# Kernel optimization log

Hardware: AMD Instinct MI355X
Metric: run time of the kernel (lower is better)

## Reference

```python
import jax, jax.numpy as jnp
import numpy as np

H = 512
IN_CH = 3
DIM = 32
FILTER_SIZES = [4, 4, 2]
OUT_DIM = 1
BATCH = 128


def _patchify(x, f):
    # (B, C, D, D) -> (B, C, P, P, f*f) non-overlapping patches (matches torch unfold+reshape)
    B, C, D, _ = x.shape
    P = D // f
    xp = x.reshape(B, C, P, f, P, f).transpose(0, 1, 2, 4, 3, 5)
    return xp.reshape(B, C, P, P, f * f)


def _loc_block(x, w, f):
    # w: (O, C, P, P, f*f) -- per-patch unshared filters
    C = x.shape[1]
    xp = _patchify(x, f)
    y = jnp.einsum('bcpqf,ocpqf->bopq', xp, w)
    return jax.nn.relu(y / (f * f * C) ** 0.5)


def setup_inputs() -> dict:
    key = jax.random.key(0)
    ks = jax.random.split(key, 5)
    f1, f2, f3 = FILTER_SIZES
    P1 = DIM // f1            # 8
    P2 = P1 // f2             # 2
    P3 = P2 // f3             # 1
    x = jax.random.normal(ks[0], (BATCH, IN_CH, DIM, DIM), dtype=jnp.float32)
    w1 = jax.random.normal(ks[1], (H, IN_CH, P1, P1, f1 * f1), dtype=jnp.float32)
    w2 = jax.random.normal(ks[2], (H, H, P2, P2, f2 * f2), dtype=jnp.float32)
    w3 = jax.random.normal(ks[3], (H, H, P3, P3, f3 * f3), dtype=jnp.float32)
    beta = jax.random.normal(ks[4], (H * P3 * P3, OUT_DIM), dtype=jnp.float32)
    return {'x': x, 'w1': w1, 'w2': w2, 'w3': w3, 'beta': beta}


def reference(x, w1, w2, w3, beta):
    f1, f2, f3 = FILTER_SIZES
    y = _loc_block(x, w1, f1)
    y = _loc_block(y, w2, f2)
    y = _loc_block(y, w3, f3)
    y = y.reshape(y.shape[0], -1)
    return y @ beta / beta.shape[0] ** 0.5
```

## Files before the change

### kernel.cpp

```cpp
#include <hip/hip_runtime.h>


typedef _Float16 f16;
typedef _Float16 half8 __attribute__((ext_vector_type(8)));
typedef _Float16 half4 __attribute__((ext_vector_type(4)));
typedef float f32x4 __attribute__((ext_vector_type(4)));

#define SWZ(r, c) ((((r) << 6) + (c)) ^ (((r) & 7) << 3))
#define SWZL(r, c) ((((r) << 10) + (c)) ^ (((r) & 7) << 3))

#define GLOAD_LDS16(G, L)                                                     \
  __builtin_amdgcn_global_load_lds(                                           \
      (const __attribute__((address_space(1))) void*)(G),                     \
      (__attribute__((address_space(3))) void*)(L), 16, 0, 0)

__global__ __launch_bounds__(256) void l1_mfma(const float* __restrict__ x,
                                               const float* __restrict__ w1,
                                               f16* __restrict__ A2) {
  const int o0 = blockIdx.x << 5;
  const int s2 = blockIdx.y;
  const int b0 = blockIdx.z << 5;
  const int p2 = s2 >> 1, q2 = s2 & 1;
  __shared__ __align__(16) f16 Xs[32 * 1024];
  __shared__ __align__(16) f16 Ws[32 * 1024];
  const int t = threadIdx.x;
#pragma unroll
  for (int i = 0; i < 8; ++i) {
    int e = (i << 8) + t;
    int row = e >> 6, rem = e & 63, g = rem >> 2, j = rem & 3;
    half4 z = {};
    *(half4*)&Xs[SWZL(row, g * 64 + 48 + j * 4)] = z;
    *(half4*)&Ws[SWZL(row, g * 64 + 48 + j * 4)] = z;
  }
#pragma unroll
  for (int i = 0; i < 24; ++i) {
    int fl = (i << 8) + t;
    int b = fl / 192, rem = fl % 192;
    int c = rem >> 6, rem2 = rem & 63;
    int a = rem2 >> 4, fi = (rem2 >> 2) & 3, bq = rem2 & 3;
    float4 v = *(const float4*)(x + ((size_t)(b0 + b) * 3 + c) * 1024 +
                                (p2 * 16 + a * 4 + fi) * 32 + q2 * 16 + bq * 4);
    half4 h;
    h[0] = (f16)v.x; h[1] = (f16)v.y; h[2] = (f16)v.z; h[3] = (f16)v.w;
    *(half4*)&Xs[SWZL(b, (a * 4 + bq) * 64 + c * 16 + fi * 4)] = h;
  }
#pragma unroll
  for (int i = 0; i < 24; ++i) {
    int fl = (i << 8) + t;
    int o = fl / 192, rem = fl % 192;
    int c = rem >> 6, rem2 = rem & 63;
    int g = rem2 >> 2, f4 = rem2 & 3;
    float4 v = *(const float4*)(w1 + (size_t)(o0 + o) * 3072 + c * 1024 +
                                (p2 * 4 + (g >> 2)) * 128 + (q2 * 4 + (g & 3)) * 16 + f4 * 4);
    half4 h;
    h[0] = (f16)v.x; h[1] = (f16)v.y; h[2] = (f16)v.z; h[3] = (f16)v.w;
    *(half4*)&Ws[SWZL(o, g * 64 + c * 16 + f4 * 4)] = h;
  }
  __syncthreads();

  const int wv = t >> 6, ln = t & 63;
  const int bw = wv >> 1, ow = wv & 1;
  const int frow = ln & 15, fr4 = ln >> 4;
  f32x4 acc[16] = {};
#pragma unroll
  for (int g = 0; g < 16; ++g) {
#pragma unroll
    for (int ks = 0; ks < 2; ++ks) {
      half8 a = *(const half8*)&Xs[SWZL(bw * 16 + frow, g * 64 + ks * 32 + fr4 * 8)];
      half8 b = *(const half8*)&Ws[SWZL(ow * 16 + frow, g * 64 + ks * 32 + fr4 * 8)];
      acc[g] = __builtin_amdgcn_mfma_f32_16x16x32_f16(a, b, acc[g], 0, 0, 0);
    }
  }
  f16* A2b = A2 + (size_t)s2 * 128 * 8192;
#pragma unroll
  for (int r = 0; r < 4; ++r) {
    int b = b0 + bw * 16 + fr4 * 4 + r;
    int o = o0 + ow * 16 + frow;
    f16 tmp[16];
#pragma unroll
    for (int g = 0; g < 16; ++g)
      tmp[g] = (f16)fmaxf(acc[g][r] * 0.14433756729740643f, 0.f);
    f16* dst = A2b + (size_t)b * 8192 + o * 16;
    *(half8*)dst = *(half8*)&tmp[0];
    *(half8*)(dst + 8) = *(half8*)&tmp[8];
  }
}

__global__ __launch_bounds__(512) void gemm0(const f16* __restrict__ A,
                                             const float* __restrict__ W,
                                             f16* __restrict__ P) {
  __shared__ __align__(16) f16 As[2][128 * 64];
  __shared__ __align__(16) float Bs[2][128 * 64];
  const int t = threadIdx.x;
  const int bid = blockIdx.x;
  constexpr int AK = 8192, ITERS = 8;
  const int s = bid >> 6;
  const int kc = (bid >> 2) & 15;
  const int n = bid & 3;
  const int kb0 = kc * (ITERS * 64);
  const f16* Ab = A + (size_t)s * 128 * AK + kb0;
  const int o0 = n << 7;

  const int wv = t >> 6, ln = t & 63;

#define STAGE(IT, BUF)                                                          \
  {                                                                             \
    _Pragma("unroll") for (int jj = 0; jj < 2; ++jj) {                          \
      int rbase = wv * 16 + jj * 8;                                             \
      int r = rbase + (ln >> 3);                                                \
      int sg = (ln & 7) ^ (r & 7);                                              \
      GLOAD_LDS16(Ab + (size_t)r * AK + ((IT) << 6) + (sg << 3),                \
                  &As[BUF][rbase << 6]);                                        \
    }                                                                           \
    _Pragma("unroll") for (int jj = 0; jj < 4; ++jj) {                          \
      int rbase = wv * 16 + jj * 4;                                             \
      int r = rbase + (ln >> 4);                                                \
      int sg = (ln & 15) ^ (r & 7);                                             \
      int k = kb0 + ((IT) << 6) + (sg << 2);                                    \
      const float* gp = W + (size_t)(o0 + r) * 32768 + ((k >> 4) << 6) +        \
                        (s << 4) + (k & 15);                                    \
      GLOAD_LDS16(gp, &Bs[BUF][rbase << 6]);                                    \
    }                                                                           \
  }

  const int wr = wv >> 2, wc = wv & 3;
  const int frow = ln & 15, fr4 = ln >> 4;
  f32x4 acc[4][2] = {};

#define COMPUTE(BUF)                                                            \
  _Pragma("unroll") for (int ks = 0; ks < 2; ++ks) {                            \
    half8 a[4];                                                                 \
    _Pragma("unroll") for (int mi = 0; mi < 4; ++mi) {                          \
      int r = wr * 64 + mi * 16 + frow;                                         \
      int gl = ((ks << 2) + fr4) ^ (r & 7);                                     \
      a[mi] = *(const half8*)&As[BUF][(r << 6) + (gl << 3)];                    \
    }                                                                           \
    _Pragma("unroll") for (int ni = 0; ni < 2; ++ni) {                          \
      int r = wc * 32 + ni * 16 + frow;                                         \
      int s0 = (ks << 3) + (fr4 << 1);                                          \
      float4 f0 = *(const float4*)&Bs[BUF][(r << 6) + ((s0 ^ (r & 7)) << 2)];   \
      float4 f1 = *(const float4*)&Bs[BUF][(r << 6) + (((s0 + 1) ^ (r & 7)) << 2)]; \
      half8 hb;                                                                 \
      hb[0] = (f16)f0.x; hb[1] = (f16)f0.y; hb[2] = (f16)f0.z; hb[3] = (f16)f0.w; \
      hb[4] = (f16)f1.x; hb[5] = (f16)f1.y; hb[6] = (f16)f1.z; hb[7] = (f16)f1.w; \
      _Pragma("unroll") for (int mi = 0; mi < 4; ++mi)                          \
        acc[mi][ni] = __builtin_amdgcn_mfma_f32_16x16x32_f16(a[mi], hb, acc[mi][ni], 0, 0, 0); \
    }                                                                           \
  }

  STAGE(0, 0)
#pragma unroll
  for (int it = 0; it < ITERS; ++it) {
    const int cur = it & 1;
    if (it + 1 < ITERS) {
      STAGE(it + 1, cur ^ 1)
      asm volatile("s_waitcnt vmcnt(6)" ::: "memory");
    } else {
      asm volatile("s_waitcnt vmcnt(0)" ::: "memory");
    }
    __builtin_amdgcn_s_barrier();
    __builtin_amdgcn_sched_barrier(0);
    COMPUTE(cur)
    __builtin_amdgcn_sched_barrier(0);
    __builtin_amdgcn_s_barrier();
  }

  f16* Pb = P + (size_t)((kc << 2) + s) * 65536;
#pragma unroll
  for (int mi = 0; mi < 4; ++mi)
#pragma unroll
    for (int ni = 0; ni < 2; ++ni)
#pragma unroll
      for (int r = 0; r < 4; ++r) {
        int gm = wr * 64 + mi * 16 + fr4 * 4 + r;
        int gn = o0 + wc * 32 + ni * 16 + frow;
        Pb[(size_t)gm * 512 + gn] = (f16)acc[mi][ni][r];
      }
#undef STAGE
#undef COMPUTE
}

__global__ __launch_bounds__(256) void gemm1(const f16* __restrict__ A,
                                             const float* __restrict__ W,
                                             f16* __restrict__ P) {
  __shared__ __align__(16) f16 As[2][128 * 64];
  __shared__ __align__(16) float Bs[2][64 * 64];
  const int t = threadIdx.x;
  const int bid = blockIdx.x;
  constexpr int AK = 2048, ITERS = 2;
  const int kc = bid >> 3;
  const int n = bid & 7;
  const int kb0 = kc * (ITERS * 64);
  const f16* Ab = A + kb0;
  const int o0 = n << 6;
  const int wv = t >> 6, ln = t & 63;
  const int a_r = (ln >> 3), a_sg0 = ln & 7;
  const int b_r = (ln >> 4), b_sg0 = ln & 15;

#define STAGE(IT, BUF)                                                          \
  {                                                                             \
    _Pragma("unroll") for (int jj = 0; jj < 4; ++jj) {                          \
      int rbase = wv * 32 + jj * 8;                                             \
      int r = rbase + a_r;                                                      \
      int sg = a_sg0 ^ (r & 7);                                                 \
      GLOAD_LDS16(Ab + (size_t)r * AK + ((IT) << 6) + (sg << 3),                \
                  &As[BUF][rbase << 6]);                                        \
    }                                                                           \
    _Pragma("unroll") for (int jj = 0; jj < 4; ++jj) {                          \
      int rbase = wv * 16 + jj * 4;                                             \
      int r = rbase + b_r;                                                      \
      int sg = b_sg0 ^ (r & 7);                                                 \
      const float* gp = W + (size_t)(o0 + r) * 2048 + kb0 + ((IT) << 6) + (sg << 2); \
      GLOAD_LDS16(gp, &Bs[BUF][rbase << 6]);                                    \
    }                                                                           \
  }

  const int wr = wv >> 1, wc = wv & 1;
  const int frow = ln & 15, fr4 = ln >> 4;
  f32x4 acc[4][2] = {};

#define COMPUTE(BUF)                                                            \
  _Pragma("unroll") for (int ks = 0; ks < 2; ++ks) {                            \
    half8 a[4];                                                                 \
    _Pragma("unroll") for (int mi = 0; mi < 4; ++mi) {                          \
      int r = wr * 64 + mi * 16 + frow;                                         \
      int gl = ((ks << 2) + fr4) ^ (r & 7);                                     \
      a[mi] = *(const half8*)&As[BUF][(r << 6) + (gl << 3)];                    \
    }                                                                           \
    _Pragma("unroll") for (int ni = 0; ni < 2; ++ni) {                          \
      int r = wc * 32 + ni * 16 + frow;                                         \
      int s0 = (ks << 3) + (fr4 << 1);                                          \
      float4 f0 = *(const float4*)&Bs[BUF][(r << 6) + ((s0 ^ (r & 7)) << 2)];   \
      float4 f1 = *(const float4*)&Bs[BUF][(r << 6) + (((s0 + 1) ^ (r & 7)) << 2)]; \
      half8 hb;                                                                 \
      hb[0] = (f16)f0.x; hb[1] = (f16)f0.y; hb[2] = (f16)f0.z; hb[3] = (f16)f0.w; \
      hb[4] = (f16)f1.x; hb[5] = (f16)f1.y; hb[6] = (f16)f1.z; hb[7] = (f16)f1.w; \
      _Pragma("unroll") for (int mi = 0; mi < 4; ++mi)                          \
        acc[mi][ni] = __builtin_amdgcn_mfma_f32_16x16x32_f16(a[mi], hb, acc[mi][ni], 0, 0, 0); \
    }                                                                           \
  }

  STAGE(0, 0)
#pragma unroll
  for (int it = 0; it < ITERS; ++it) {
    const int cur = it & 1;
    if (it + 1 < ITERS) {
      STAGE(it + 1, cur ^ 1)
      asm volatile("s_waitcnt vmcnt(8)" ::: "memory");
    } else {
      asm volatile("s_waitcnt vmcnt(0)" ::: "memory");
    }
    __builtin_amdgcn_s_barrier();
    __builtin_amdgcn_sched_barrier(0);
    COMPUTE(cur)
    __builtin_amdgcn_sched_barrier(0);
    __builtin_amdgcn_s_barrier();
  }

  f16* Pb = P + (size_t)kc * 65536;
#pragma unroll
  for (int mi = 0; mi < 4; ++mi)
#pragma unroll
    for (int ni = 0; ni < 2; ++ni)
#pragma unroll
      for (int r = 0; r < 4; ++r) {
        int gm = wr * 64 + mi * 16 + fr4 * 4 + r;
        int gn = o0 + wc * 32 + ni * 16 + frow;
        Pb[(size_t)gm * 512 + gn] = (f16)acc[mi][ni][r];
      }
#undef STAGE
#undef COMPUTE
}

__global__ __launch_bounds__(256) void reduce2(const f16* __restrict__ P2,
                                               f16* __restrict__ A3) {
  int idx = blockIdx.x * 256 + threadIdx.x;
  int og = idx & 127, b = idx >> 7;
  f16 outv[16];
#pragma unroll
  for (int s = 0; s < 4; ++s) {
    float a0 = 0.f, a1 = 0.f, a2 = 0.f, a3 = 0.f;
#pragma unroll
    for (int kc = 0; kc < 16; ++kc) {
      half4 v = *(const half4*)(P2 + (size_t)((kc << 2) + s) * 65536 + b * 512 + og * 4);
      a0 += (float)v[0]; a1 += (float)v[1]; a2 += (float)v[2]; a3 += (float)v[3];
    }
    outv[0 * 4 + s] = (f16)fmaxf(a0 * 0.011048543456039805f, 0.f);
    outv[1 * 4 + s] = (f16)fmaxf(a1 * 0.011048543456039805f, 0.f);
    outv[2 * 4 + s] = (f16)fmaxf(a2 * 0.011048543456039805f, 0.f);
    outv[3 * 4 + s] = (f16)fmaxf(a3 * 0.011048543456039805f, 0.f);
  }
  f16* dst = A3 + (size_t)b * 2048 + og * 16;
  *(half8*)dst = *(half8*)&outv[0];
  *(half8*)(dst + 8) = *(half8*)&outv[8];
}

__global__ __launch_bounds__(256) void out_fused(const f16* __restrict__ P3,
                                                 const float* __restrict__ beta,
                                                 float* __restrict__ out) {
  __shared__ float red[4];
  const int b = blockIdx.x, t = threadIdx.x;
  float acc = 0.f;
#pragma unroll
  for (int oi = 0; oi < 2; ++oi) {
    int o = (oi << 8) + t;
    float v = 0.f;
#pragma unroll
    for (int kc = 0; kc < 16; ++kc) v += (float)P3[(size_t)kc * 65536 + b * 512 + o];
    acc += fmaxf(v * 0.022097086912079608f, 0.f) * beta[o];
  }
#pragma unroll
  for (int off = 32; off > 0; off >>= 1) acc += __shfl_down(acc, off);
  if ((t & 63) == 0) red[t >> 6] = acc;
  __syncthreads();
  if (t == 0) out[b] = (red[0] + red[1] + red[2] + red[3]) * 0.044194173824159216f;
}

extern "C" void kernel_launch(void* const* d_in, const int* in_sizes, int n_in,
                              void* d_out, int out_size, void* d_ws, size_t ws_size,
                              hipStream_t stream) {
  const float* x    = (const float*)d_in[0];
  const float* w1   = (const float*)d_in[1];
  const float* w2   = (const float*)d_in[2];
  const float* w3   = (const float*)d_in[3];
  const float* beta = (const float*)d_in[4];
  float* out = (float*)d_out;

  char* wsb = (char*)d_ws;
  f16* A2 = (f16*)wsb;
  f16* P2 = (f16*)(wsb + (8ull << 20));
  f16* A3 = (f16*)(wsb + (16ull << 20));
  f16* P3 = (f16*)(wsb + (16ull << 20) + (1ull << 19));

  l1_mfma<<<dim3(16, 4, 4), 256, 0, stream>>>(x, w1, A2);
  gemm0<<<256, 512, 0, stream>>>(A2, w2, P2);
  reduce2<<<64, 256, 0, stream>>>(P2, A3);
  gemm1<<<128, 256, 0, stream>>>(A3, w3, P3);
  out_fused<<<128, 256, 0, stream>>>(P3, beta, out);
}
```

Before: 44.98 us.

## Stage gemm0 B weights via registers with fp16 conversion before LDS write

gemm0 used to DMA fp32 weights straight into LDS and convert them to fp16 inside the MFMA inner loop. Now each thread loads the weights as float4 into registers, converts them to half4 once, and writes them into a swizzled fp16 LDS buffer after the compute of the current stage. This halves the LDS footprint of B and takes the conversion out of the per-MFMA path, and launch bounds add an occupancy hint. The cost is extra VGPRs for the staged registers and a register round-trip that may overlap less well with compute than the direct-to-LDS DMA did.

```diff
diff --git a/kernel.cpp b/kernel.cpp
--- a/kernel.cpp
+++ b/kernel.cpp
@@ -86,41 +86,50 @@
   }
 }
 
-__global__ __launch_bounds__(512) void gemm0(const f16* __restrict__ A,
-                                             const float* __restrict__ W,
-                                             f16* __restrict__ P) {
+__global__ __launch_bounds__(512, 4) void gemm0(const f16* __restrict__ A,
+                                                const float* __restrict__ W,
+                                                f16* __restrict__ P) {
   __shared__ __align__(16) f16 As[2][128 * 64];
-  __shared__ __align__(16) float Bs[2][128 * 64];
+  __shared__ __align__(16) f16 Bs[2][128 * 64];
   const int t = threadIdx.x;
   const int bid = blockIdx.x;
   constexpr int AK = 8192, ITERS = 8;
   const int s = bid >> 6;
   const int kc = (bid >> 2) & 15;
   const int n = bid & 3;
-  const int kb0 = kc * (ITERS * 64);
+  const int kb0 = kc * 512;
   const f16* Ab = A + (size_t)s * 128 * AK + kb0;
   const int o0 = n << 7;
 
   const int wv = t >> 6, ln = t & 63;
-
-#define STAGE(IT, BUF)                                                          \
-  {                                                                             \
-    _Pragma("unroll") for (int jj = 0; jj < 2; ++jj) {                          \
-      int rbase = wv * 16 + jj * 8;                                             \
-      int r = rbase + (ln >> 3);                                                \
-      int sg = (ln & 7) ^ (r & 7);                                              \
-      GLOAD_LDS16(Ab + (size_t)r * AK + ((IT) << 6) + (sg << 3),                \
-                  &As[BUF][rbase << 6]);                                        \
-    }                                                                           \
-    _Pragma("unroll") for (int jj = 0; jj < 4; ++jj) {                          \
-      int rbase = wv * 16 + jj * 4;                                             \
-      int r = rbase + (ln >> 4);                                                \
-      int sg = (ln & 15) ^ (r & 7);                                             \
-      int k = kb0 + ((IT) << 6) + (sg << 2);                                    \
-      const float* gp = W + (size_t)(o0 + r) * 32768 + ((k >> 4) << 6) +        \
-                        (s << 4) + (k & 15);                                    \
-      GLOAD_LDS16(gp, &Bs[BUF][rbase << 6]);                                    \
-    }                                                                           \
+  const int br = t >> 4, bslot = t & 15;
+  float4 breg[4];
+
+#define B_LOAD(IT)                                                              \
+  _Pragma("unroll") for (int i = 0; i < 4; ++i) {                               \
+    int r = i * 32 + br;                                                        \
+    int k = kb0 + ((IT) << 6) + (bslot << 2);                                   \
+    breg[i] = *(const float4*)(W + (size_t)(o0 + r) * 32768 + ((k >> 4) << 6) + \
+                               (s << 4) + (k & 15));                            \
+  }
+
+#define A_DMA(IT, BUF)                                                          \
+  _Pragma("unroll") for (int jj = 0; jj < 2; ++jj) {                            \
+    int rbase = wv * 16 + jj * 8;                                               \
+    int r = rbase + (ln >> 3);                                                  \
+    int sg = (ln & 7) ^ (r & 7);                                                \
+    GLOAD_LDS16(Ab + (size_t)r * AK + ((IT) << 6) + (sg << 3),                  \
+                &As[BUF][rbase << 6]);                                          \
+  }
+
+#define B_WRITE(BUF)                                                            \
+  _Pragma("unroll") for (int i = 0; i < 4; ++i) {                               \
+    int r = i * 32 + br;                                                        \
+    half4 h4;                                                                   \
+    h4[0] = (f16)breg[i].x; h4[1] = (f16)breg[i].y;                             \
+    h4[2] = (f16)breg[i].z; h4[3] = (f16)breg[i].w;                             \
+    int off = (r << 6) + (((bslot >> 1) ^ (r & 7)) << 3) + ((bslot & 1) << 2);  \
+    *(half4*)&Bs[BUF][off] = h4;                                                \
   }
 
   const int wr = wv >> 2, wc = wv & 3;
@@ -137,31 +146,35 @@
     }                                                                           \
     _Pragma("unroll") for (int ni = 0; ni < 2; ++ni) {                          \
       int r = wc * 32 + ni * 16 + frow;                                         \
-      int s0 = (ks << 3) + (fr4 << 1);                                          \
-      float4 f0 = *(const float4*)&Bs[BUF][(r << 6) + ((s0 ^ (r & 7)) << 2)];   \
-      float4 f1 = *(const float4*)&Bs[BUF][(r << 6) + (((s0 + 1) ^ (r & 7)) << 2)]; \
-      half8 hb;                                                                 \
-      hb[0] = (f16)f0.x; hb[1] = (f16)f0.y; hb[2] = (f16)f0.z; hb[3] = (f16)f0.w; \
-      hb[4] = (f16)f1.x; hb[5] = (f16)f1.y; hb[6] = (f16)f1.z; hb[7] = (f16)f1.w; \
+      int gl = ((ks << 2) + fr4) ^ (r & 7);                                     \
+      half8 hb = *(const half8*)&Bs[BUF][(r << 6) + (gl << 3)];                 \
       _Pragma("unroll") for (int mi = 0; mi < 4; ++mi)                          \
         acc[mi][ni] = __builtin_amdgcn_mfma_f32_16x16x32_f16(a[mi], hb, acc[mi][ni], 0, 0, 0); \
     }                                                                           \
   }
 
-  STAGE(0, 0)
+  B_LOAD(0)
+  A_DMA(0, 0)
+  asm volatile("s_waitcnt vmcnt(2)" ::: "memory");
+  B_WRITE(0)
 #pragma unroll
   for (int it = 0; it < ITERS; ++it) {
     const int cur = it & 1;
     if (it + 1 < ITERS) {
-      STAGE(it + 1, cur ^ 1)
-      asm volatile("s_waitcnt vmcnt(6)" ::: "memory");
+      B_LOAD(it + 1)
+      A_DMA(it + 1, cur ^ 1)
+      asm volatile("s_waitcnt vmcnt(6) lgkmcnt(0)" ::: "memory");
     } else {
-      asm volatile("s_waitcnt vmcnt(0)" ::: "memory");
+      asm volatile("s_waitcnt vmcnt(0) lgkmcnt(0)" ::: "memory");
     }
     __builtin_amdgcn_s_barrier();
     __builtin_amdgcn_sched_barrier(0);
     COMPUTE(cur)
     __builtin_amdgcn_sched_barrier(0);
+    if (it + 1 < ITERS) {
+      asm volatile("s_waitcnt vmcnt(2)" ::: "memory");
+      B_WRITE(cur ^ 1)
+    }
     __builtin_amdgcn_s_barrier();
   }
 
@@ -176,7 +189,9 @@
         int gn = o0 + wc * 32 + ni * 16 + frow;
         Pb[(size_t)gm * 512 + gn] = (f16)acc[mi][ni][r];
       }
-#undef STAGE
+#undef B_LOAD
+#undef A_DMA
+#undef B_WRITE
 #undef COMPUTE
 }
 
```

Result: no change. 45.31 us (+0.7%).
